# Kernel optimization log

Measured on AMD Instinct MI355X. Metric: run time of the kernel, lower is better.

## Reference

```python
import jax, jax.numpy as jnp
import numpy as np


def _conv(x, w, b, pad):
    y = jax.lax.conv_general_dilated(
        x, w, window_strides=(1, 1), padding=[(pad, pad), (pad, pad)],
        dimension_numbers=('NCHW', 'OIHW', 'NCHW'))
    return y + b[None, :, None, None]


def _deform_conv2d(x, offsets, mask, w, b):
    # x: [B,C,H,W]; offsets: [B,2*K,H,W] (dy,dx pairs per kernel tap, row-major taps);
    # mask: [B,K,H,W]; w: [O,C,3,3]; stride=1, padding=1 (torchvision semantics).
    B, C, H, W = x.shape
    K = 9
    off = offsets.reshape(B, K, 2, H, W)
    dy, dx = off[:, :, 0], off[:, :, 1]                      # [B,K,H,W]
    ky = (jnp.arange(K) // 3 - 1).astype(x.dtype)            # tap row offset (pad=1)
    kx = (jnp.arange(K) % 3 - 1).astype(x.dtype)             # tap col offset
    hh = jnp.arange(H, dtype=x.dtype)
    ww = jnp.arange(W, dtype=x.dtype)
    py = hh[None, None, :, None] + ky[None, :, None, None] + dy   # sample y, [B,K,H,W]
    px = ww[None, None, None, :] + kx[None, :, None, None] + dx   # sample x
    y0 = jnp.floor(py); x0 = jnp.floor(px)
    wy = py - y0;      wx = px - x0
    y0i = y0.astype(jnp.int32); x0i = x0.astype(jnp.int32)
    xflat = x.reshape(B, C, H * W)

    def gather(yy, xx):
        # zero padding outside the feature map (torchvision behavior)
        valid = ((yy >= 0) & (yy < H) & (xx >= 0) & (xx < W)).astype(x.dtype)
        idx = jnp.clip(yy, 0, H - 1) * W + jnp.clip(xx, 0, W - 1)
        idx = jnp.broadcast_to(idx.reshape(B, 1, K * H * W), (B, C, K * H * W))
        g = jnp.take_along_axis(xflat, idx, axis=2).reshape(B, C, K, H, W)
        return g * valid[:, None]

    sampled = (gather(y0i, x0i)         * ((1 - wy) * (1 - wx))[:, None]
             + gather(y0i, x0i + 1)     * ((1 - wy) * wx)[:, None]
             + gather(y0i + 1, x0i)     * (wy * (1 - wx))[:, None]
             + gather(y0i + 1, x0i + 1) * (wy * wx)[:, None])       # [B,C,K,H,W]
    sampled = sampled * mask[:, None]                                # modulation
    out = jnp.einsum('bckhw,ock->bohw', sampled, w.reshape(w.shape[0], C, K))
    return out + b[None, :, None, None]


def setup_inputs() -> dict:
    key = jax.random.key(0)
    ks = jax.random.split(key, 5)
    B, C, Ht, Wt, Hs, Ws = 4, 256, 32, 32, 64, 64
    return {
        'template_feat': jax.random.normal(ks[0], (B, C, Ht, Wt), jnp.float32),
        'search_feat':   jax.random.normal(ks[1], (B, C, Hs, Ws), jnp.float32),
        'offset_w': jax.random.normal(ks[2], (18, 2 * C, 3, 3), jnp.float32) * 0.01,
        'offset_b': jnp.zeros((18,), jnp.float32),
        'mask_w':   jax.random.normal(ks[3], (9, 2 * C, 1, 1), jnp.float32) * 0.06,
        'mask_b':   jnp.zeros((9,), jnp.float32),
        'deform_w': jax.random.normal(ks[4], (C, C, 3, 3), jnp.float32) * 0.03,
        'deform_b': jnp.zeros((C,), jnp.float32),
    }


def reference(template_feat, search_feat, offset_w, offset_b, mask_w, mask_b, deform_w, deform_b):
    B, C, Hs, Ws = search_feat.shape
    # F.interpolate(..., mode='bilinear', align_corners=False) == jax half-pixel bilinear
    aligned = jax.image.resize(template_feat, (B, C, Hs, Ws), method='bilinear')
    combined = jnp.concatenate([aligned, search_feat], axis=1)       # [B,2C,H,W]
    offsets = _conv(combined, offset_w, offset_b, 1)                 # [B,18,H,W]
    mask = jax.nn.sigmoid(_conv(combined, mask_w, mask_b, 0))        # [B,9,H,W]
    return _deform_conv2d(search_feat, offsets, mask, deform_w, deform_b)
```

## Files before the change

### kernel.cpp

```cpp
#include <hip/hip_runtime.h>
#include <math.h>

#define BB 4
#define CC 256
#define HH 64
#define WW 64
#define HW 4096
#define XTR 4240
#define XPAD 72

typedef __attribute__((ext_vector_type(8))) _Float16 half8;
typedef __attribute__((ext_vector_type(4))) _Float16 half4;
typedef __attribute__((ext_vector_type(4))) float f32x4;

__device__ inline void gld16(const void* g, void* l) {
    __builtin_amdgcn_global_load_lds((const __attribute__((address_space(1))) void*)g,
                                     (__attribute__((address_space(3))) void*)l, 16, 0, 0);
}

__global__ __launch_bounds__(256) void prep_kernel(
    const float* __restrict__ tmpl, const float* __restrict__ search,
    const float* __restrict__ ow, const float* __restrict__ mw,
    const float* __restrict__ dw,
    _Float16* __restrict__ XT, _Float16* __restrict__ W2, _Float16* __restrict__ W3T) {
    int blk = blockIdx.x;
    int tid = threadIdx.x;
    __shared__ _Float16 ts[64 * 72];
    __shared__ float ts2[64 * 64];

    if (blk < 2048) {
        int ct = blk & 7, y = (blk >> 3) & 63, b = blk >> 9;
        if (ct >= 4) {
            const float* sp = search + ((size_t)(b * CC + (ct - 4) * 64) * HW) + y * 64;
#pragma unroll
            for (int it = 0; it < 4; ++it) {
                int c_l = it * 16 + (tid >> 4);
                int x4 = tid & 15;
                float4 v = *(const float4*)(sp + (size_t)c_l * HW + x4 * 4);
                half4 h;
                h.x = (_Float16)v.x; h.y = (_Float16)v.y;
                h.z = (_Float16)v.z; h.w = (_Float16)v.w;
                *(half4*)&ts[c_l * 72 + x4 * 4] = h;
            }
        } else {
            float sy = 0.5f * (float)y - 0.25f;
            float fy = floorf(sy);
            float wy = sy - fy;
            int y0 = (int)fy;
            int y0c = min(max(y0, 0), 31), y1c = min(max(y0 + 1, 0), 31);
            const float* tp0 = tmpl + ((size_t)(b * CC + ct * 64) * 1024);
#pragma unroll
            for (int j = 0; j < 4; ++j) {
                int idx = j * 256 + tid;
                int c_l = idx >> 4;
                int row = (idx >> 3) & 1;
                int w4 = idx & 7;
                const float* src = tp0 + (size_t)c_l * 1024 + (row ? y1c : y0c) * 32 + w4 * 4;
                *(float4*)&ts2[c_l * 64 + row * 32 + w4 * 4] = *(const float4*)src;
            }
            __syncthreads();
#pragma unroll 4
            for (int it = 0; it < 16; ++it) {
                int c_l = it * 4 + (tid >> 6);
                int x = tid & 63;
                float sx = 0.5f * (float)x - 0.25f;
                float fx = floorf(sx);
                float wx = sx - fx;
                int x0 = (int)fx;
                int x0c = min(max(x0, 0), 31), x1c = min(max(x0 + 1, 0), 31);
                float v00 = ts2[c_l * 64 + x0c], v01 = ts2[c_l * 64 + x1c];
                float v10 = ts2[c_l * 64 + 32 + x0c], v11 = ts2[c_l * 64 + 32 + x1c];
                ts[c_l * 72 + x] = (_Float16)((1.f - wy) * ((1.f - wx) * v00 + wx * v01) +
                                              wy * ((1.f - wx) * v10 + wx * v11));
            }
        }
        __syncthreads();
        size_t rowbase = (size_t)b * XTR + XPAD + (size_t)y * 64;
        for (int it = 0; it < 2; ++it) {
            int idx = it * 256 + tid;
            int x = idx >> 3, w = idx & 7;
            half8 o;
#pragma unroll
            for (int j = 0; j < 8; ++j) o[j] = ts[(w * 8 + j) * 72 + x];
            *(half8*)&XT[(rowbase + x) * 512 + ct * 64 + ((w ^ (x & 7)) * 8)] = o;
        }
    } else if (blk < 2192) {
        int idx = (blk - 2048) * 256 + tid;
        int w = idx & 63;
        int r = (idx >> 6) % 144;
        int b = idx / 9216;
        int pr = (r < 72) ? r : (r + 4096);
        half8 z = {};
        *(half8*)&XT[((size_t)b * XTR + pr) * 512 + w * 8] = z;
    } else if (blk < 2264) {
        int idx = (blk - 2192) * 256 + tid;
        int q = idx & 7;
        int oc = (idx >> 3) & 31;
        int tap = (idx >> 8) % 9;
        int ch = idx / 2304;
        int c0 = ch * 64 + (q ^ (oc & 7)) * 8;
        half8 o;
#pragma unroll
        for (int j = 0; j < 8; ++j) {
            int c = c0 + j;
            float v = 0.f;
            if (oc < 18) v = ow[((size_t)oc * 512 + c) * 9 + tap];
            else if (oc < 27 && tap == 4) v = mw[(size_t)(oc - 18) * 512 + c];
            o[j] = (_Float16)v;
        }
        *(half8*)&W2[(size_t)idx * 8] = o;
    } else {
        int g = (blk - 2264) * 256 + tid;
        int ot = g / 36864;
        int rem = g - ot * 36864;
        int ks = rem >> 10;
        int ci = rem & 1023;
        int r = ci >> 3, q = ci & 7;
        int qs = q ^ (r & 7);
        int o_ = ot * 128 + r;
        int kc0 = ks * 64 + qs * 8;
        half8 o;
#pragma unroll
        for (int j = 0; j < 8; ++j) {
            int kc = kc0 + j;
            int k = kc >> 8, c = kc & 255;
            o[j] = (_Float16)dw[((size_t)o_ * CC + c) * 9 + k];
        }
        *(half8*)&W3T[(size_t)g * 8] = o;
    }
}

__global__ __launch_bounds__(512) void offsample_kernel(
    const _Float16* __restrict__ XT, const _Float16* __restrict__ W2,
    const float* __restrict__ ob, const float* __restrict__ mb,
    _Float16* __restrict__ ST2) {
    int orig = blockIdx.x;
    int blk = ((orig & 7) << 5) + (orig >> 3);
    int b = blk >> 6, pt = blk & 63;
    int p0 = pt * 64;
    int tid = threadIdx.x, wave = tid >> 6, lane = tid & 63;
    int l15 = lane & 15, kq = lane >> 4;
    int grp = wave >> 2;
    int w4 = wave & 3;
    int tid256 = tid & 255;

    __shared__ __align__(16) char smem[124928];
    _Float16* A_s = (_Float16*)(smem + grp * 62464);
    _Float16* B_s = (_Float16*)(smem + grp * 62464 + 36864);
    float* red_s = (float*)smem;
    float* offs_s = (float*)(smem + 8192);
    ushort4* r4 = (ushort4*)(smem + 15104);
    float4* wg4 = (float4*)(smem + 19712);

    f32x4 acc[2];
    acc[0] = (f32x4){0.f, 0.f, 0.f, 0.f};
    acc[1] = (f32x4){0.f, 0.f, 0.f, 0.f};

    const char* xrow = (const char*)(XT + ((size_t)b * XTR + XPAD + p0 - 65) * 512);
    half8 z8 = {};
    int x_ = w4 * 16 + l15;

    for (int ch4 = 0; ch4 < 4; ++ch4) {
        int ch = grp * 4 + ch4;
        __syncthreads();
        const char* srcA = (const char*)W2 + (size_t)ch * 36864;
#pragma unroll
        for (int it = 0; it < 9; ++it) {
            int b16 = it * 256 + w4 * 64;
            gld16(srcA + (size_t)(b16 + lane) * 16, (char*)A_s + b16 * 16);
        }
#pragma unroll
        for (int it = 0; it < 7; ++it) {
            int b16 = it * 256 + w4 * 64;
            if (b16 < 1552) {
                int c16 = b16 + lane;
                int r_u = c16 >> 3, q = c16 & 7;
                gld16(xrow + (size_t)r_u * 1024 + ch * 128 + q * 16, (char*)B_s + b16 * 16);
            }
        }
        __syncthreads();

#pragma unroll
        for (int tap = 0; tap < 9; ++tap) {
            int ky = tap / 3 - 1, kx = tap % 3 - 1;
            int dlt = ky * 64 + kx;
            int key = (l15 + dlt + 72) & 7;
            bool iv0 = (kx == -1 && x_ == 0) || (kx == 1 && x_ == 63);
            int r0 = w4 * 16 + l15 + 65 + dlt;
#pragma unroll
            for (int ks = 0; ks < 2; ++ks) {
                int qa = ((ks * 4 + kq) ^ (l15 & 7)) * 8;
                int qb = ((ks * 4 + kq) ^ key) * 8;
                half8 fa0 = *(const half8*)&A_s[tap * 2048 + l15 * 64 + qa];
                half8 fa1 = *(const half8*)&A_s[tap * 2048 + (16 + l15) * 64 + qa];
                half8 fb0 = *(const half8*)&B_s[r0 * 64 + qb];
                if (iv0) fb0 = z8;
                acc[0] = __builtin_amdgcn_mfma_f32_16x16x32_f16(fa0, fb0, acc[0], 0, 0, 0);
                acc[1] = __builtin_amdgcn_mfma_f32_16x16x32_f16(fa1, fb0, acc[1], 0, 0, 0);
            }
        }
    }

    __syncthreads();
    if (grp == 1) {
#pragma unroll
        for (int m = 0; m < 2; ++m)
#pragma unroll
            for (int r = 0; r < 4; ++r)
                red_s[(m * 4 + r) * 256 + tid256] = acc[m][r];
    }
    __syncthreads();
    if (grp == 0) {
#pragma unroll
        for (int m = 0; m < 2; ++m) {
#pragma unroll
            for (int r = 0; r < 4; ++r) {
                int oc = m * 16 + kq * 4 + r;
                float v = acc[m][r] + red_s[(m * 4 + r) * 256 + tid256];
                if (oc < 18) {
                    offs_s[oc * 64 + x_] = v + ob[oc];
                } else if (oc < 27) {
                    float s = v + mb[oc - 18];
                    offs_s[oc * 64 + x_] = 1.f / (1.f + expf(-s));
                }
            }
        }
    }
    __syncthreads();

    for (int i = tid; i < 576; i += 512) {
        int k = i >> 6, t = i & 63;
        int p = p0 + t;
        int y = p >> 6, x = p & 63;
        float dy = offs_s[(2 * k) * 64 + t];
        float dx = offs_s[(2 * k + 1) * 64 + t];
        float m = offs_s[(18 + k) * 64 + t];
        float py = (float)(y + k / 3 - 1) + dy;
        float px = (float)(x + k % 3 - 1) + dx;
        float fy0 = floorf(py), fx0 = floorf(px);
        float wy = py - fy0, wx = px - fx0;
        int y0 = (int)fy0, x0 = (int)fx0;
        bool vy0 = (y0 >= 0) && (y0 < HH);
        bool vy1 = (y0 + 1 >= 0) && (y0 + 1 < HH);
        bool vx0 = (x0 >= 0) && (x0 < WW);
        bool vx1 = (x0 + 1 >= 0) && (x0 + 1 < WW);
        float w00 = (vy0 && vx0) ? (1.f - wy) * (1.f - wx) * m : 0.f;
        float w01 = (vy0 && vx1) ? (1.f - wy) * wx * m : 0.f;
        float w10 = (vy1 && vx0) ? wy * (1.f - wx) * m : 0.f;
        float w11 = (vy1 && vx1) ? wy * wx * m : 0.f;
        int y0c = min(max(y0, 0), HH - 1), y1c = min(max(y0 + 1, 0), HH - 1);
        int x0c = min(max(x0, 0), WW - 1), x1c = min(max(x0 + 1, 0), WW - 1);
        r4[i] = make_ushort4((ushort)(y0c * 64 + x0c), (ushort)(y0c * 64 + x1c),
                             (ushort)(y1c * 64 + x0c), (ushort)(y1c * 64 + x1c));
        wg4[i] = make_float4(w00, w01, w10, w11);
    }
    __syncthreads();

    const _Float16* xb = XT + ((size_t)b * XTR + XPAD) * 512;
    int oct = tid & 31;
    int gg64 = (4 + (oct >> 3)) * 64;
    int w0 = oct & 7;
    size_t tb = ((size_t)(b * 32 + (pt >> 1))) * 36;
    int rbase = (pt & 1) * 64;

    for (int k = 0; k < 9; ++k) {
        int ks36 = k * 4 + (oct >> 3);
#pragma unroll
        for (int it = 0; it < 4; ++it) {
            int p_l = it * 16 + (tid >> 5);
            ushort4 rr = r4[k * 64 + p_l];
            float4 w = wg4[k * 64 + p_l];
            half8 c00 = *(const half8*)(xb + (size_t)rr.x * 512 + gg64 + ((w0 ^ (rr.x & 7)) * 8));
            half8 c01 = *(const half8*)(xb + (size_t)rr.y * 512 + gg64 + ((w0 ^ (rr.y & 7)) * 8));
            half8 c10 = *(const half8*)(xb + (size_t)rr.z * 512 + gg64 + ((w0 ^ (rr.z & 7)) * 8));
            half8 c11 = *(const half8*)(xb + (size_t)rr.w * 512 + gg64 + ((w0 ^ (rr.w & 7)) * 8));
            half8 o;
#pragma unroll
            for (int j = 0; j < 8; ++j) {
                float v = w.x * (float)c00[j] + w.y * (float)c01[j] +
                          w.z * (float)c10[j] + w.w * (float)c11[j];
                o[j] = (_Float16)v;
            }
            int r = rbase + p_l;
            *(half8*)&ST2[((tb + ks36) << 13) + (r * 8 + (w0 ^ (r & 7))) * 8] = o;
        }
    }
}

__global__ __launch_bounds__(512) void deform_mfma(
    const _Float16* __restrict__ W3T, const _Float16* __restrict__ ST2,
    const float* __restrict__ db, float* __restrict__ out) {
    int orig = blockIdx.x;
    int xq = orig & 7, j = orig >> 3;
    int b = xq >> 1;
    int ot = j >> 4;
    int pt = ((xq & 1) << 4) + (j & 15);
    int o0 = ot * 128, p0 = pt * 128;
    int tid = threadIdx.x;
    int wave = tid >> 6, lane = tid & 63;
    int wo = (wave & 1) * 64, wp = (wave >> 1) * 32;

    __shared__ __align__(16) _Float16 As[4][8192];
    __shared__ __align__(16) _Float16 Bs[4][8192];

    f32x4 acc[4][2];
#pragma unroll
    for (int i = 0; i < 4; ++i)
#pragma unroll
        for (int j2 = 0; j2 < 2; ++j2) acc[i][j2] = (f32x4){0.f, 0.f, 0.f, 0.f};

    const _Float16* Asrc = W3T + (size_t)ot * (36 * 8192);
    const _Float16* Bsrc = ST2 + ((size_t)(b * 32 + pt)) * (36 * 8192);
    int fr = lane & 15, kq8 = lane >> 4;

    auto stage = [&](int buf, int ks) {
#pragma unroll
        for (int t = 0; t < 2; ++t) {
            int ci = t * 512 + tid;
            gld16(Asrc + (((size_t)ks) << 13) + (size_t)ci * 8,
                  (char*)&As[buf][0] + (size_t)ci * 16);
        }
#pragma unroll
        for (int t = 0; t < 2; ++t) {
            int ci = t * 512 + tid;
            gld16(Bsrc + (((size_t)ks) << 13) + (size_t)ci * 8,
                  (char*)&Bs[buf][0] + (size_t)ci * 16);
        }
    };

    auto compute = [&](int cur) {
        __builtin_amdgcn_s_setprio(1);
#pragma unroll
        for (int ks2 = 0; ks2 < 2; ++ks2) {
            int c8 = ks2 * 4 + kq8;
            int cho = (c8 ^ (fr & 7)) * 8;
            half8 fa[4], fb[2];
#pragma unroll
            for (int f = 0; f < 4; ++f)
                fa[f] = *(const half8*)&As[cur][(wo + f * 16 + fr) * 64 + cho];
#pragma unroll
            for (int g = 0; g < 2; ++g)
                fb[g] = *(const half8*)&Bs[cur][(wp + g * 16 + fr) * 64 + cho];
#pragma unroll
            for (int i = 0; i < 4; ++i)
#pragma unroll
                for (int j2 = 0; j2 < 2; ++j2)
                    acc[i][j2] = __builtin_amdgcn_mfma_f32_16x16x32_f16(fa[i], fb[j2], acc[i][j2], 0, 0, 0);
        }
        __builtin_amdgcn_s_setprio(0);
    };

    stage(0, 0);
    stage(1, 1);
    stage(2, 2);

    for (int m = 0; m < 8; ++m) {
#pragma unroll
        for (int u = 0; u < 4; ++u) {
            int ks = m * 4 + u;
            asm volatile("s_waitcnt vmcnt(8)" ::: "memory");
            __builtin_amdgcn_s_barrier();
            asm volatile("" ::: "memory");
            compute(u);
            stage((u + 3) & 3, ks + 3);
        }
    }
    asm volatile("s_waitcnt vmcnt(8)" ::: "memory");
    __builtin_amdgcn_s_barrier();
    asm volatile("" ::: "memory");
    compute(0);
    stage(3, 35);
    asm volatile("s_waitcnt vmcnt(8)" ::: "memory");
    __builtin_amdgcn_s_barrier();
    asm volatile("" ::: "memory");
    compute(1);
    asm volatile("s_waitcnt vmcnt(4)" ::: "memory");
    __builtin_amdgcn_s_barrier();
    asm volatile("" ::: "memory");
    compute(2);
    asm volatile("s_waitcnt vmcnt(0)" ::: "memory");
    __builtin_amdgcn_s_barrier();
    asm volatile("" ::: "memory");
    compute(3);

    int col = lane & 15, rb = (lane >> 4) * 4;
#pragma unroll
    for (int i = 0; i < 4; ++i) {
        int o_ = o0 + wo + i * 16 + rb;
#pragma unroll
        for (int j2 = 0; j2 < 2; ++j2) {
            int p_ = p0 + wp + j2 * 16 + col;
#pragma unroll
            for (int r = 0; r < 4; ++r) {
                out[((size_t)(b * CC + o_ + r)) * HW + p_] = acc[i][j2][r] + db[o_ + r];
            }
        }
    }
}

extern "C" void kernel_launch(void* const* d_in, const int* in_sizes, int n_in,
                              void* d_out, int out_size, void* d_ws, size_t ws_size,
                              hipStream_t stream) {
    const float* tmpl = (const float*)d_in[0];
    const float* search = (const float*)d_in[1];
    const float* ow = (const float*)d_in[2];
    const float* ob = (const float*)d_in[3];
    const float* mw = (const float*)d_in[4];
    const float* mb = (const float*)d_in[5];
    const float* dw = (const float*)d_in[6];
    const float* db = (const float*)d_in[7];
    float* out = (float*)d_out;

    _Float16* XTp = (_Float16*)d_ws;
    _Float16* W2 = XTp + (size_t)4 * XTR * 512;
    _Float16* W3T = W2 + 147456;
    _Float16* ST2 = W3T + 589824;

    prep_kernel<<<2552, 256, 0, stream>>>(tmpl, search, ow, mw, dw, XTp, W2, W3T);
    offsample_kernel<<<256, 512, 0, stream>>>(XTp, W2, ob, mb, ST2);
    deform_mfma<<<256, 512, 0, stream>>>(W3T, ST2, db, out);
}
```

Before: 71.15 us.

## Drop split-K channel groups in offset conv; use single group of four waves

The offset/mask conv stage previously split the 8 channel chunks across two groups of four waves, each with its own LDS tile, and summed the partials through shared memory. Now only the first 256 threads run all 8 chunks serially, so LDS drops to about 62KB and the cross-group reduction and its barrier go away. This may let more blocks fit per CU, but it halves the waves working on the MFMA stage while the other 256 threads sit idle until the sampling phase.

```diff
diff --git a/kernel.cpp b/kernel.cpp
--- a/kernel.cpp
+++ b/kernel.cpp
@@ -140,17 +140,13 @@
     int p0 = pt * 64;
     int tid = threadIdx.x, wave = tid >> 6, lane = tid & 63;
     int l15 = lane & 15, kq = lane >> 4;
-    int grp = wave >> 2;
-    int w4 = wave & 3;
-    int tid256 = tid & 255;
-
-    __shared__ __align__(16) char smem[124928];
-    _Float16* A_s = (_Float16*)(smem + grp * 62464);
-    _Float16* B_s = (_Float16*)(smem + grp * 62464 + 36864);
-    float* red_s = (float*)smem;
-    float* offs_s = (float*)(smem + 8192);
-    ushort4* r4 = (ushort4*)(smem + 15104);
-    float4* wg4 = (float4*)(smem + 19712);
+
+    __shared__ __align__(16) char smem[62464];
+    _Float16* A_s = (_Float16*)smem;
+    _Float16* B_s = (_Float16*)(smem + 36864);
+    float* offs_s = (float*)smem;
+    ushort4* r4 = (ushort4*)(smem + 6912);
+    float4* wg4 = (float4*)(smem + 11520);
 
     f32x4 acc[2];
     acc[0] = (f32x4){0.f, 0.f, 0.f, 0.f};
@@ -158,65 +154,60 @@
 
     const char* xrow = (const char*)(XT + ((size_t)b * XTR + XPAD + p0 - 65) * 512);
     half8 z8 = {};
-    int x_ = w4 * 16 + l15;
-
-    for (int ch4 = 0; ch4 < 4; ++ch4) {
-        int ch = grp * 4 + ch4;
+    int x_ = wave * 16 + l15;
+
+    for (int ch = 0; ch < 8; ++ch) {
         __syncthreads();
-        const char* srcA = (const char*)W2 + (size_t)ch * 36864;
-#pragma unroll
-        for (int it = 0; it < 9; ++it) {
-            int b16 = it * 256 + w4 * 64;
-            gld16(srcA + (size_t)(b16 + lane) * 16, (char*)A_s + b16 * 16);
-        }
-#pragma unroll
-        for (int it = 0; it < 7; ++it) {
-            int b16 = it * 256 + w4 * 64;
-            if (b16 < 1552) {
-                int c16 = b16 + lane;
-                int r_u = c16 >> 3, q = c16 & 7;
-                gld16(xrow + (size_t)r_u * 1024 + ch * 128 + q * 16, (char*)B_s + b16 * 16);
+        if (tid < 256) {
+            const char* srcA = (const char*)W2 + (size_t)ch * 36864;
+#pragma unroll
+            for (int it = 0; it < 9; ++it) {
+                int b16 = it * 256 + wave * 64;
+                gld16(srcA + (size_t)(b16 + lane) * 16, (char*)A_s + b16 * 16);
+            }
+#pragma unroll
+            for (int it = 0; it < 7; ++it) {
+                int b16 = it * 256 + wave * 64;
+                if (b16 < 1552) {
+                    int c16 = b16 + lane;
+                    int r_u = c16 >> 3, q = c16 & 7;
+                    gld16(xrow + (size_t)r_u * 1024 + ch * 128 + q * 16, (char*)B_s + b16 * 16);
+                }
             }
         }
         __syncthreads();
 
-#pragma unroll
-        for (int tap = 0; tap < 9; ++tap) {
-            int ky = tap / 3 - 1, kx = tap % 3 - 1;
-            int dlt = ky * 64 + kx;
-            int key = (l15 + dlt + 72) & 7;
-            bool iv0 = (kx == -1 && x_ == 0) || (kx == 1 && x_ == 63);
-            int r0 = w4 * 16 + l15 + 65 + dlt;
-#pragma unroll
-            for (int ks = 0; ks < 2; ++ks) {
-                int qa = ((ks * 4 + kq) ^ (l15 & 7)) * 8;
-                int qb = ((ks * 4 + kq) ^ key) * 8;
-                half8 fa0 = *(const half8*)&A_s[tap * 2048 + l15 * 64 + qa];
-                half8 fa1 = *(const half8*)&A_s[tap * 2048 + (16 + l15) * 64 + qa];
-                half8 fb0 = *(const half8*)&B_s[r0 * 64 + qb];
-                if (iv0) fb0 = z8;
-                acc[0] = __builtin_amdgcn_mfma_f32_16x16x32_f16(fa0, fb0, acc[0], 0, 0, 0);
-                acc[1] = __builtin_amdgcn_mfma_f32_16x16x32_f16(fa1, fb0, acc[1], 0, 0, 0);
+        if (tid < 256) {
+#pragma unroll
+            for (int tap = 0; tap < 9; ++tap) {
+                int ky = tap / 3 - 1, kx = tap % 3 - 1;
+                int dlt = ky * 64 + kx;
+                int key = (l15 + dlt + 72) & 7;
+                bool iv0 = (kx == -1 && x_ == 0) || (kx == 1 && x_ == 63);
+                int r0 = wave * 16 + l15 + 65 + dlt;
+#pragma unroll
+                for (int ks = 0; ks < 2; ++ks) {
+                    int qa = ((ks * 4 + kq) ^ (l15 & 7)) * 8;
+                    int qb = ((ks * 4 + kq) ^ key) * 8;
+                    half8 fa0 = *(const half8*)&A_s[tap * 2048 + l15 * 64 + qa];
+                    half8 fa1 = *(const half8*)&A_s[tap * 2048 + (16 + l15) * 64 + qa];
+                    half8 fb0 = *(const half8*)&B_s[r0 * 64 + qb];
+                    if (iv0) fb0 = z8;
+                    acc[0] = __builtin_amdgcn_mfma_f32_16x16x32_f16(fa0, fb0, acc[0], 0, 0, 0);
+                    acc[1] = __builtin_amdgcn_mfma_f32_16x16x32_f16(fa1, fb0, acc[1], 0, 0, 0);
+                }
             }
         }
     }
 
     __syncthreads();
-    if (grp == 1) {
-#pragma unroll
-        for (int m = 0; m < 2; ++m)
-#pragma unroll
-            for (int r = 0; r < 4; ++r)
-                red_s[(m * 4 + r) * 256 + tid256] = acc[m][r];
-    }
-    __syncthreads();
-    if (grp == 0) {
+    if (tid < 256) {
 #pragma unroll
         for (int m = 0; m < 2; ++m) {
 #pragma unroll
             for (int r = 0; r < 4; ++r) {
                 int oc = m * 16 + kq * 4 + r;
-                float v = acc[m][r] + red_s[(m * 4 + r) * 256 + tid256];
+                float v = acc[m][r];
                 if (oc < 18) {
                     offs_s[oc * 64 + x_] = v + ob[oc];
                 } else if (oc < 27) {
```

After: 74.89 us. +5.2%, slower.

## Halve deform GEMM pixel tile to 64 and double grid with 3-stage pipeline

Applied to the files above, without the earlier changes.

Shrinks the deform_mfma output tile from 128x128 to 128x64 pixels, which doubles the grid to 512 blocks so more of the GPU's compute units get work. The LDS pipeline drops from 4 to 3 stages and per-step B staging is halved, which cuts shared memory per block. Each wave now issues 4 MFMAs per k-substep instead of 8. The A (weight) tile is loaded twice as often overall, and the shallower pipeline may hide less latency.

```diff
diff --git a/kernel.cpp b/kernel.cpp
--- a/kernel.cpp
+++ b/kernel.cpp
@@ -293,24 +293,23 @@
     int orig = blockIdx.x;
     int xq = orig & 7, j = orig >> 3;
     int b = xq >> 1;
-    int ot = j >> 4;
-    int pt = ((xq & 1) << 4) + (j & 15);
-    int o0 = ot * 128, p0 = pt * 128;
+    int hi = xq & 1;
+    int ot = j >> 5;
+    int pt = hi * 32 + (j & 31);
+    int o0 = ot * 128, p0 = pt * 64;
     int tid = threadIdx.x;
     int wave = tid >> 6, lane = tid & 63;
-    int wo = (wave & 1) * 64, wp = (wave >> 1) * 32;
-
-    __shared__ __align__(16) _Float16 As[4][8192];
-    __shared__ __align__(16) _Float16 Bs[4][8192];
-
-    f32x4 acc[4][2];
-#pragma unroll
-    for (int i = 0; i < 4; ++i)
-#pragma unroll
-        for (int j2 = 0; j2 < 2; ++j2) acc[i][j2] = (f32x4){0.f, 0.f, 0.f, 0.f};
+    int wo = (wave & 1) * 64, wp = (wave >> 1) * 16;
+
+    __shared__ __align__(16) _Float16 As[3][8192];
+    __shared__ __align__(16) _Float16 Bs[3][4096];
+
+    f32x4 acc[4];
+#pragma unroll
+    for (int i = 0; i < 4; ++i) acc[i] = (f32x4){0.f, 0.f, 0.f, 0.f};
 
     const _Float16* Asrc = W3T + (size_t)ot * (36 * 8192);
-    const _Float16* Bsrc = ST2 + ((size_t)(b * 32 + pt)) * (36 * 8192);
+    const _Float16* Bsrc = ST2 + ((size_t)(b * 32 + (pt >> 1))) * (36 * 8192) + (pt & 1) * 4096;
     int fr = lane & 15, kq8 = lane >> 4;
 
     auto stage = [&](int buf, int ks) {
@@ -320,12 +319,8 @@
             gld16(Asrc + (((size_t)ks) << 13) + (size_t)ci * 8,
                   (char*)&As[buf][0] + (size_t)ci * 16);
         }
-#pragma unroll
-        for (int t = 0; t < 2; ++t) {
-            int ci = t * 512 + tid;
-            gld16(Bsrc + (((size_t)ks) << 13) + (size_t)ci * 8,
-                  (char*)&Bs[buf][0] + (size_t)ci * 16);
-        }
+        gld16(Bsrc + (((size_t)ks) << 13) + (size_t)tid * 8,
+              (char*)&Bs[buf][0] + (size_t)tid * 16);
     };
 
     auto compute = [&](int cur) {
@@ -334,66 +329,54 @@
         for (int ks2 = 0; ks2 < 2; ++ks2) {
             int c8 = ks2 * 4 + kq8;
             int cho = (c8 ^ (fr & 7)) * 8;
-            half8 fa[4], fb[2];
+            half8 fa[4], fb;
 #pragma unroll
             for (int f = 0; f < 4; ++f)
                 fa[f] = *(const half8*)&As[cur][(wo + f * 16 + fr) * 64 + cho];
-#pragma unroll
-            for (int g = 0; g < 2; ++g)
-                fb[g] = *(const half8*)&Bs[cur][(wp + g * 16 + fr) * 64 + cho];
+            fb = *(const half8*)&Bs[cur][(wp + fr) * 64 + cho];
 #pragma unroll
             for (int i = 0; i < 4; ++i)
-#pragma unroll
-                for (int j2 = 0; j2 < 2; ++j2)
-                    acc[i][j2] = __builtin_amdgcn_mfma_f32_16x16x32_f16(fa[i], fb[j2], acc[i][j2], 0, 0, 0);
+                acc[i] = __builtin_amdgcn_mfma_f32_16x16x32_f16(fa[i], fb, acc[i], 0, 0, 0);
         }
         __builtin_amdgcn_s_setprio(0);
     };
 
     stage(0, 0);
     stage(1, 1);
-    stage(2, 2);
-
-    for (int m = 0; m < 8; ++m) {
-#pragma unroll
-        for (int u = 0; u < 4; ++u) {
-            int ks = m * 4 + u;
-            asm volatile("s_waitcnt vmcnt(8)" ::: "memory");
+
+    for (int m = 0; m < 11; ++m) {
+#pragma unroll
+        for (int u = 0; u < 3; ++u) {
+            int ks = m * 3 + u;
+            asm volatile("s_waitcnt vmcnt(3)" ::: "memory");
             __builtin_amdgcn_s_barrier();
             asm volatile("" ::: "memory");
             compute(u);
-            stage((u + 3) & 3, ks + 3);
-        }
-    }
-    asm volatile("s_waitcnt vmcnt(8)" ::: "memory");
+            stage((u + 2) % 3, ks + 2);
+        }
+    }
+    asm volatile("s_waitcnt vmcnt(3)" ::: "memory");
     __builtin_amdgcn_s_barrier();
     asm volatile("" ::: "memory");
     compute(0);
-    stage(3, 35);
-    asm volatile("s_waitcnt vmcnt(8)" ::: "memory");
+    stage(2, 35);
+    asm volatile("s_waitcnt vmcnt(3)" ::: "memory");
     __builtin_amdgcn_s_barrier();
     asm volatile("" ::: "memory");
     compute(1);
-    asm volatile("s_waitcnt vmcnt(4)" ::: "memory");
+    asm volatile("s_waitcnt vmcnt(0)" ::: "memory");
     __builtin_amdgcn_s_barrier();
     asm volatile("" ::: "memory");
     compute(2);
-    asm volatile("s_waitcnt vmcnt(0)" ::: "memory");
-    __builtin_amdgcn_s_barrier();
-    asm volatile("" ::: "memory");
-    compute(3);
 
     int col = lane & 15, rb = (lane >> 4) * 4;
 #pragma unroll
     for (int i = 0; i < 4; ++i) {
         int o_ = o0 + wo + i * 16 + rb;
-#pragma unroll
-        for (int j2 = 0; j2 < 2; ++j2) {
-            int p_ = p0 + wp + j2 * 16 + col;
-#pragma unroll
-            for (int r = 0; r < 4; ++r) {
-                out[((size_t)(b * CC + o_ + r)) * HW + p_] = acc[i][j2][r] + db[o_ + r];
-            }
+        int p_ = p0 + wp + col;
+#pragma unroll
+        for (int r = 0; r < 4; ++r) {
+            out[((size_t)(b * CC + o_ + r)) * HW + p_] = acc[i][r] + db[o_ + r];
         }
     }
 }
@@ -418,5 +401,5 @@
 
     prep_kernel<<<2552, 256, 0, stream>>>(tmpl, search, ow, mw, dw, XTp, W2, W3T);
     offsample_kernel<<<256, 512, 0, stream>>>(XTp, W2, ob, mb, ST2);
-    deform_mfma<<<256, 512, 0, stream>>>(W3T, ST2, db, out);
+    deform_mfma<<<512, 512, 0, stream>>>(W3T, ST2, db, out);
 }
```

Result: slower. 74.72 us (+5.0%).
